# Kernel optimization log

Measured on AMD Instinct MI355X. Metric: run time of the kernel, lower is better.

## Reference

```python
import jax, jax.numpy as jnp
import numpy as np

N_HOS, N_TYP, N_STRUCTS = 2, 3, 8
N_COMBOS = N_HOS * N_TYP  # 6
BATCH = 32768
N_ITERS = 150  # PDHG iterations to solve the per-sample QP

S_NP = np.array([[1,0,0,1,0,1,0,0],
                 [0,1,0,1,0,0,1,0],
                 [0,0,1,0,1,0,0,1],
                 [1,0,0,0,1,1,0,0],
                 [0,1,0,0,0,0,1,1],
                 [0,0,1,1,1,0,0,0]], dtype=np.float32)


def setup_inputs() -> dict:
    key = jax.random.key(0)
    ks = jax.random.split(key, 10)
    def lin(kw, fan_in, fan_out):
        lim = 1.0 / np.sqrt(fan_in)
        kw1, kw2 = jax.random.split(kw)
        W = jax.random.uniform(kw1, (fan_out, fan_in), jnp.float32, -lim, lim)
        b = jax.random.uniform(kw2, (fan_out,), jnp.float32, -lim, lim)
        return W, b
    W1, b1 = lin(ks[0], 6, 20)
    W2, b2 = lin(ks[1], 20, 20)
    W3, b3 = lin(ks[2], 20, 20)
    W4, b4 = lin(ks[3], 20, 8)
    X = jax.random.uniform(ks[4], (BATCH, N_HOS, N_TYP), jnp.float32)  # nonneg bids -> feasible QP (x=0)
    return {"X": X, "W1": W1, "b1": b1, "W2": W2, "b2": b2, "W3": W3, "b3": b3,
            "W4": W4, "b4": b4, "S": jnp.asarray(S_NP), "batch_size": BATCH}


def _solve_qp(z, b, S):
    """Batched PDHG for: max w.x - ||x-z||_2  s.t. x>=0, S x <= b, with w = 1.
    z: [B, ns], b: [B, m], S: [m, ns]. Returns x: [B, ns]."""
    B, ns = z.shape
    m = S.shape[0]
    w = jnp.ones_like(z)
    # K = [S; -I]; Frobenius bound on spectral norm (safe step sizes)
    L = jnp.sqrt(jnp.sum(S * S) + ns)
    tau = 0.9 / L
    sigma = 0.9 / L

    def prox_f(u):
        # prox of tau*(||x-z|| - w.x) at u  (closed form: shifted norm shrinkage)
        v = u + tau * w - z
        nv = jnp.linalg.norm(v, axis=-1, keepdims=True)
        scale = jnp.maximum(1.0 - tau / jnp.maximum(nv, 1e-12), 0.0)
        return z + scale * v

    def step(carry, _):
        x, l1, l2 = carry
        x_new = prox_f(x - tau * (l1 @ S - l2))  # K^T lam = S^T l1 - l2
        xbar = 2.0 * x_new - x
        l1n = jnp.maximum(l1 + sigma * (xbar @ S.T) - sigma * b, 0.0)  # dual of Sx<=b
        l2n = jnp.maximum(l2 - sigma * xbar, 0.0)                      # dual of -x<=0
        return (x_new, l1n, l2n), None

    x0 = jnp.maximum(z, 0.0)
    l1 = jnp.zeros((B, m), z.dtype)
    l2 = jnp.zeros((B, ns), z.dtype)
    (x, _, _), _ = jax.lax.scan(step, (x0, l1, l2), None, length=N_ITERS)
    return x


def reference(X, W1, b1, W2, b2, W3, b3, W4, b4, S, batch_size):
    B = X.shape[0]
    Z = X.reshape(B, -1)                       # [B, 6] = bids flattened (also the QP rhs b)
    h = jnp.tanh(Z @ W1.T + b1)
    h = jnp.tanh(h @ W2.T + b2)
    h = jnp.tanh(h @ W3.T + b3)
    z = jnp.tanh(h @ W4.T + b4)                # [B, 8] anchor point for QP
    return _solve_qp(z, Z, S)                  # [B, 8] allocation
```

## Files before the change

kernel.cpp:

```cpp
#include <hip/hip_runtime.h>
#include <math.h>


#define NITERS 150

__device__ __forceinline__ float ftanh(float a) {
    float e = __expf(2.0f * a);
    return fmaf(-2.0f, __builtin_amdgcn_rcpf(e + 1.0f), 1.0f);
}

__global__ __launch_bounds__(64) void matchnet_kernel(
    const float* __restrict__ X,
    const float* __restrict__ W1, const float* __restrict__ b1,
    const float* __restrict__ W2, const float* __restrict__ b2,
    const float* __restrict__ W3, const float* __restrict__ b3,
    const float* __restrict__ W4, const float* __restrict__ b4,
    float* __restrict__ out, int B)
{
    __shared__ float sw[1148];
    const int t = threadIdx.x;
    for (int i = t; i < 120; i += 64) sw[i]        = W1[i];
    for (int i = t; i < 20;  i += 64) sw[120 + i]  = b1[i];
    for (int i = t; i < 400; i += 64) sw[140 + i]  = W2[i];
    for (int i = t; i < 20;  i += 64) sw[540 + i]  = b2[i];
    for (int i = t; i < 400; i += 64) sw[560 + i]  = W3[i];
    for (int i = t; i < 20;  i += 64) sw[960 + i]  = b3[i];
    for (int i = t; i < 160; i += 64) sw[980 + i]  = W4[i];
    if (t < 8) sw[1140 + t] = b4[t];
    __syncthreads();

    const int gid = blockIdx.x * 64 + t;
    if (gid >= B) return;

    const float TAU = 0.9f / sqrtf(26.0f);
    const float SIG = TAU;

    float zin[6];
    {
        const float2* xp = (const float2*)(X + (size_t)gid * 6);
        float2 p0 = xp[0], p1 = xp[1], p2 = xp[2];
        zin[0] = p0.x; zin[1] = p0.y; zin[2] = p1.x;
        zin[3] = p1.y; zin[4] = p2.x; zin[5] = p2.y;
    }

    float h1[20];
#pragma unroll
    for (int j = 0; j < 20; ++j) {
        float a = sw[120 + j];
#pragma unroll
        for (int k = 0; k < 6; ++k) a = fmaf(sw[j*6 + k], zin[k], a);
        h1[j] = ftanh(a);
    }
    float h2[20];
#pragma unroll
    for (int j = 0; j < 20; ++j) {
        float a = sw[540 + j];
#pragma unroll
        for (int k = 0; k < 20; ++k) a = fmaf(sw[140 + j*20 + k], h1[k], a);
        h2[j] = ftanh(a);
    }
    float h3[20];
#pragma unroll
    for (int j = 0; j < 20; ++j) {
        float a = sw[960 + j];
#pragma unroll
        for (int k = 0; k < 20; ++k) a = fmaf(sw[560 + j*20 + k], h2[k], a);
        h3[j] = ftanh(a);
    }
    float z[8];
#pragma unroll
    for (int j = 0; j < 8; ++j) {
        float a = sw[1140 + j];
#pragma unroll
        for (int k = 0; k < 20; ++k) a = fmaf(sw[980 + j*20 + k], h3[k], a);
        z[j] = ftanh(a);
    }

    float x[8], l2[8], tz[8];
#pragma unroll
    for (int j = 0; j < 8; ++j) { x[j] = fmaxf(z[j], 0.0f); l2[j] = 0.0f; tz[j] = TAU - z[j]; }
    float l1[6], sb[6];
#pragma unroll
    for (int i = 0; i < 6; ++i) { l1[i] = 0.0f; sb[i] = SIG * zin[i]; }

#pragma unroll 1
    for (int it = 0; it < NITERS; ++it) {
        float t03 = l1[0] + l1[3];
        float t14 = l1[1] + l1[4];
        float t25 = l1[2] + l1[5];
        float st[8];
        st[0] = t03; st[1] = t14; st[2] = t25;
        st[3] = (l1[0] + l1[1]) + l1[5];
        st[4] = (l1[2] + l1[3]) + l1[5];
        st[5] = t03; st[6] = t14;
        st[7] = l1[2] + l1[4];

        float v[8];
#pragma unroll
        for (int j = 0; j < 8; ++j)
            v[j] = fmaf(-TAU, st[j] - l2[j], x[j]) + tz[j];

        float n01 = fmaf(v[0], v[0], v[1]*v[1]);
        float n23 = fmaf(v[2], v[2], v[3]*v[3]);
        float n45 = fmaf(v[4], v[4], v[5]*v[5]);
        float n67 = fmaf(v[6], v[6], v[7]*v[7]);
        float nv2 = (n01 + n23) + (n45 + n67);
        float scale = fmaxf(fmaf(-TAU, __builtin_amdgcn_rsqf(nv2), 1.0f), 0.0f);

        float xb[8];
#pragma unroll
        for (int j = 0; j < 8; ++j) {
            float xn = fmaf(scale, v[j], z[j]);
            xb[j] = fmaf(2.0f, xn, -x[j]);
            x[j] = xn;
            l2[j] = fmaxf(fmaf(-SIG, xb[j], l2[j]), 0.0f);
        }

        float r0 = (xb[0] + xb[3]) + xb[5];
        float r1 = (xb[1] + xb[3]) + xb[6];
        float r2 = (xb[2] + xb[4]) + xb[7];
        float r3 = (xb[0] + xb[4]) + xb[5];
        float r4 = (xb[1] + xb[6]) + xb[7];
        float r5 = (xb[2] + xb[3]) + xb[4];
        l1[0] = fmaxf(fmaf(SIG, r0, l1[0]) - sb[0], 0.0f);
        l1[1] = fmaxf(fmaf(SIG, r1, l1[1]) - sb[1], 0.0f);
        l1[2] = fmaxf(fmaf(SIG, r2, l1[2]) - sb[2], 0.0f);
        l1[3] = fmaxf(fmaf(SIG, r3, l1[3]) - sb[3], 0.0f);
        l1[4] = fmaxf(fmaf(SIG, r4, l1[4]) - sb[4], 0.0f);
        l1[5] = fmaxf(fmaf(SIG, r5, l1[5]) - sb[5], 0.0f);
    }

    float4* op = (float4*)(out + (size_t)gid * 8);
    op[0] = make_float4(x[0], x[1], x[2], x[3]);
    op[1] = make_float4(x[4], x[5], x[6], x[7]);
}

extern "C" void kernel_launch(void* const* d_in, const int* in_sizes, int n_in,
                              void* d_out, int out_size, void* d_ws, size_t ws_size,
                              hipStream_t stream) {
    const float* X  = (const float*)d_in[0];
    const float* W1 = (const float*)d_in[1];
    const float* b1 = (const float*)d_in[2];
    const float* W2 = (const float*)d_in[3];
    const float* b2 = (const float*)d_in[4];
    const float* W3 = (const float*)d_in[5];
    const float* b3 = (const float*)d_in[6];
    const float* W4 = (const float*)d_in[7];
    const float* b4 = (const float*)d_in[8];
    float* out = (float*)d_out;
    const int B = in_sizes[0] / 6;
    const int blocks = (B + 63) / 64;
    hipLaunchKernelGGL(matchnet_kernel, dim3(blocks), dim3(64), 0, stream,
                       X, W1, b1, W2, b2, W3, b3, W4, b4, out, B);
}
```

Before: 118.9 us.

## Rewrite PDHG loop in shifted variables and read MLP weights as uniform loads

Drops the shared-memory weight staging and the barrier, so weights are read straight from global memory, where uniform indices let the compiler use scalar loads. The MLP dot products become tree-shaped FMA chains built from macros. The PDHG iteration is rewritten in shifted variables (x - z + tau, l2 scaled by tau), which removes per-iteration operations from the loop-carried dependency chain. It also sets waves_per_eu(1,1), which allows more registers but can cap occupancy and hurt latency hiding.

```diff
diff --git a/kernel.cpp b/kernel.cpp
--- a/kernel.cpp
+++ b/kernel.cpp
@@ -9,7 +9,24 @@
     return fmaf(-2.0f, __builtin_amdgcn_rcpf(e + 1.0f), 1.0f);
 }
 
-__global__ __launch_bounds__(64) void matchnet_kernel(
+#define FOR20(M) M(0) M(1) M(2) M(3) M(4) M(5) M(6) M(7) M(8) M(9) \
+                 M(10) M(11) M(12) M(13) M(14) M(15) M(16) M(17) M(18) M(19)
+#define FOR8(M)  M(0) M(1) M(2) M(3) M(4) M(5) M(6) M(7)
+#define FOR6(M)  M(0) M(1) M(2) M(3) M(4) M(5)
+
+#define DOT20(W, base, H) \
+  ( (fmaf(W[(base)+0],H##0,  fmaf(W[(base)+1],H##1,  fmaf(W[(base)+2],H##2,  fmaf(W[(base)+3],H##3,  W[(base)+4]*H##4)))) \
+   + fmaf(W[(base)+5],H##5,  fmaf(W[(base)+6],H##6,  fmaf(W[(base)+7],H##7,  fmaf(W[(base)+8],H##8,  W[(base)+9]*H##9))))) \
+  + (fmaf(W[(base)+10],H##10, fmaf(W[(base)+11],H##11, fmaf(W[(base)+12],H##12, fmaf(W[(base)+13],H##13, W[(base)+14]*H##14)))) \
+   + fmaf(W[(base)+15],H##15, fmaf(W[(base)+16],H##16, fmaf(W[(base)+17],H##17, fmaf(W[(base)+18],H##18, W[(base)+19]*H##19))))) )
+
+#define DOT6(W, base, P) \
+  ( fmaf(W[(base)+0],P##0, fmaf(W[(base)+1],P##1, W[(base)+2]*P##2)) \
+  + fmaf(W[(base)+3],P##3, fmaf(W[(base)+4],P##4, W[(base)+5]*P##5)) )
+
+__global__ __launch_bounds__(64)
+__attribute__((amdgpu_waves_per_eu(1, 1), amdgpu_flat_work_group_size(64, 64)))
+void matchnet_kernel(
     const float* __restrict__ X,
     const float* __restrict__ W1, const float* __restrict__ b1,
     const float* __restrict__ W2, const float* __restrict__ b2,
@@ -17,122 +34,92 @@
     const float* __restrict__ W4, const float* __restrict__ b4,
     float* __restrict__ out, int B)
 {
-    __shared__ float sw[1148];
-    const int t = threadIdx.x;
-    for (int i = t; i < 120; i += 64) sw[i]        = W1[i];
-    for (int i = t; i < 20;  i += 64) sw[120 + i]  = b1[i];
-    for (int i = t; i < 400; i += 64) sw[140 + i]  = W2[i];
-    for (int i = t; i < 20;  i += 64) sw[540 + i]  = b2[i];
-    for (int i = t; i < 400; i += 64) sw[560 + i]  = W3[i];
-    for (int i = t; i < 20;  i += 64) sw[960 + i]  = b3[i];
-    for (int i = t; i < 160; i += 64) sw[980 + i]  = W4[i];
-    if (t < 8) sw[1140 + t] = b4[t];
-    __syncthreads();
-
-    const int gid = blockIdx.x * 64 + t;
+    const int gid = blockIdx.x * 64 + threadIdx.x;
     if (gid >= B) return;
 
     const float TAU = 0.9f / sqrtf(26.0f);
     const float SIG = TAU;
+    const float TS  = TAU * SIG;
 
-    float zin[6];
+    float zin0, zin1, zin2, zin3, zin4, zin5;
     {
         const float2* xp = (const float2*)(X + (size_t)gid * 6);
         float2 p0 = xp[0], p1 = xp[1], p2 = xp[2];
-        zin[0] = p0.x; zin[1] = p0.y; zin[2] = p1.x;
-        zin[3] = p1.y; zin[4] = p2.x; zin[5] = p2.y;
+        zin0 = p0.x; zin1 = p0.y; zin2 = p1.x;
+        zin3 = p1.y; zin4 = p2.x; zin5 = p2.y;
     }
 
-    float h1[20];
-#pragma unroll
-    for (int j = 0; j < 20; ++j) {
-        float a = sw[120 + j];
-#pragma unroll
-        for (int k = 0; k < 6; ++k) a = fmaf(sw[j*6 + k], zin[k], a);
-        h1[j] = ftanh(a);
-    }
-    float h2[20];
-#pragma unroll
-    for (int j = 0; j < 20; ++j) {
-        float a = sw[540 + j];
-#pragma unroll
-        for (int k = 0; k < 20; ++k) a = fmaf(sw[140 + j*20 + k], h1[k], a);
-        h2[j] = ftanh(a);
-    }
-    float h3[20];
-#pragma unroll
-    for (int j = 0; j < 20; ++j) {
-        float a = sw[960 + j];
-#pragma unroll
-        for (int k = 0; k < 20; ++k) a = fmaf(sw[560 + j*20 + k], h2[k], a);
-        h3[j] = ftanh(a);
-    }
-    float z[8];
-#pragma unroll
-    for (int j = 0; j < 8; ++j) {
-        float a = sw[1140 + j];
-#pragma unroll
-        for (int k = 0; k < 20; ++k) a = fmaf(sw[980 + j*20 + k], h3[k], a);
-        z[j] = ftanh(a);
-    }
+#define L1ROW(j) float h1_##j = ftanh(b1[j] + DOT6(W1, (j)*6, zin));
+    FOR20(L1ROW)
+#define L2ROW(j) float h2_##j = ftanh(b2[j] + DOT20(W2, (j)*20, h1_));
+    FOR20(L2ROW)
+#define L3ROW(j) float h3_##j = ftanh(b3[j] + DOT20(W3, (j)*20, h2_));
+    FOR20(L3ROW)
+#define ZROW(j)  float z##j  = ftanh(b4[j] + DOT20(W4, (j)*20, h3_));
+    FOR8(ZROW)
 
-    float x[8], l2[8], tz[8];
-#pragma unroll
-    for (int j = 0; j < 8; ++j) { x[j] = fmaxf(z[j], 0.0f); l2[j] = 0.0f; tz[j] = TAU - z[j]; }
-    float l1[6], sb[6];
-#pragma unroll
-    for (int i = 0; i < 6; ++i) { l1[i] = 0.0f; sb[i] = SIG * zin[i]; }
+#define INIT8(j) \
+    float zpt##j = z##j + TAU; \
+    float xz##j  = fmaxf(z##j, 0.0f) - z##j + TAU; \
+    float q##j   = 0.0f; \
+    float p##j   = xz##j;
+    FOR8(INIT8)
+
+#define INIT6(i) float l1_##i = 0.0f; float sb##i = SIG * zin##i;
+    FOR6(INIT6)
 
 #pragma unroll 1
     for (int it = 0; it < NITERS; ++it) {
-        float t03 = l1[0] + l1[3];
-        float t14 = l1[1] + l1[4];
-        float t25 = l1[2] + l1[5];
-        float st[8];
-        st[0] = t03; st[1] = t14; st[2] = t25;
-        st[3] = (l1[0] + l1[1]) + l1[5];
-        st[4] = (l1[2] + l1[3]) + l1[5];
-        st[5] = t03; st[6] = t14;
-        st[7] = l1[2] + l1[4];
+        float t03 = l1_0 + l1_3;
+        float t14 = l1_1 + l1_4;
+        float t25 = l1_2 + l1_5;
+        float st3 = (l1_0 + l1_1) + l1_5;
+        float st4 = (l1_2 + l1_3) + l1_5;
+        float st7 = l1_2 + l1_4;
 
-        float v[8];
-#pragma unroll
-        for (int j = 0; j < 8; ++j)
-            v[j] = fmaf(-TAU, st[j] - l2[j], x[j]) + tz[j];
+        float v0 = fmaf(-TAU, t03, p0);
+        float v1 = fmaf(-TAU, t14, p1);
+        float v2 = fmaf(-TAU, t25, p2);
+        float v3 = fmaf(-TAU, st3, p3);
+        float v4 = fmaf(-TAU, st4, p4);
+        float v5 = fmaf(-TAU, t03, p5);
+        float v6 = fmaf(-TAU, t14, p6);
+        float v7 = fmaf(-TAU, st7, p7);
 
-        float n01 = fmaf(v[0], v[0], v[1]*v[1]);
-        float n23 = fmaf(v[2], v[2], v[3]*v[3]);
-        float n45 = fmaf(v[4], v[4], v[5]*v[5]);
-        float n67 = fmaf(v[6], v[6], v[7]*v[7]);
+#define ZX(j) float zx##j = zpt##j - xz##j;
+        FOR8(ZX)
+
+        float n01 = fmaf(v0, v0, v1*v1);
+        float n23 = fmaf(v2, v2, v3*v3);
+        float n45 = fmaf(v4, v4, v5*v5);
+        float n67 = fmaf(v6, v6, v7*v7);
         float nv2 = (n01 + n23) + (n45 + n67);
         float scale = fmaxf(fmaf(-TAU, __builtin_amdgcn_rsqf(nv2), 1.0f), 0.0f);
+        float ss2 = scale + scale;
 
-        float xb[8];
-#pragma unroll
-        for (int j = 0; j < 8; ++j) {
-            float xn = fmaf(scale, v[j], z[j]);
-            xb[j] = fmaf(2.0f, xn, -x[j]);
-            x[j] = xn;
-            l2[j] = fmaxf(fmaf(-SIG, xb[j], l2[j]), 0.0f);
-        }
+#define UPD8(j) \
+        float xb##j = fmaf(ss2, v##j, zx##j); \
+        xz##j = fmaf(scale, v##j, TAU); \
+        q##j  = fmaxf(fmaf(-TS, xb##j, q##j), 0.0f); \
+        p##j  = xz##j + q##j;
+        FOR8(UPD8)
 
-        float r0 = (xb[0] + xb[3]) + xb[5];
-        float r1 = (xb[1] + xb[3]) + xb[6];
-        float r2 = (xb[2] + xb[4]) + xb[7];
-        float r3 = (xb[0] + xb[4]) + xb[5];
-        float r4 = (xb[1] + xb[6]) + xb[7];
-        float r5 = (xb[2] + xb[3]) + xb[4];
-        l1[0] = fmaxf(fmaf(SIG, r0, l1[0]) - sb[0], 0.0f);
-        l1[1] = fmaxf(fmaf(SIG, r1, l1[1]) - sb[1], 0.0f);
-        l1[2] = fmaxf(fmaf(SIG, r2, l1[2]) - sb[2], 0.0f);
-        l1[3] = fmaxf(fmaf(SIG, r3, l1[3]) - sb[3], 0.0f);
-        l1[4] = fmaxf(fmaf(SIG, r4, l1[4]) - sb[4], 0.0f);
-        l1[5] = fmaxf(fmaf(SIG, r5, l1[5]) - sb[5], 0.0f);
+        float r0 = (xb0 + xb3) + xb5;
+        float r1 = (xb1 + xb3) + xb6;
+        float r2 = (xb2 + xb4) + xb7;
+        float r3 = (xb0 + xb4) + xb5;
+        float r4 = (xb1 + xb6) + xb7;
+        float r5 = (xb2 + xb3) + xb4;
+
+#define L1UPD(i) l1_##i = fmaxf(fmaf(SIG, r##i, l1_##i) - sb##i, 0.0f);
+        L1UPD(0) L1UPD(1) L1UPD(2) L1UPD(3) L1UPD(4) L1UPD(5)
     }
 
     float4* op = (float4*)(out + (size_t)gid * 8);
-    op[0] = make_float4(x[0], x[1], x[2], x[3]);
-    op[1] = make_float4(x[4], x[5], x[6], x[7]);
+    op[0] = make_float4(xz0 + z0 - TAU, xz1 + z1 - TAU,
+                        xz2 + z2 - TAU, xz3 + z3 - TAU);
+    op[1] = make_float4(xz4 + z4 - TAU, xz5 + z5 - TAU,
+                        xz6 + z6 - TAU, xz7 + z7 - TAU);
 }
 
 extern "C" void kernel_launch(void* const* d_in, const int* in_sizes, int n_in,
```

After: 116.5 us. 2.0% less time.
